# Kernel tuning notes

Measured on AMD Instinct MI355X. Metric: run time of the kernel, lower is better.

The kernel has to match this reference:

```python
import jax, jax.numpy as jnp
import numpy as np

N = 200000   # residue nodes
E = 800000   # backbone edges
P = 500000   # contact pairs to score
DIN = 128    # in_channels['res']
H = 256      # hidden per layer
L = 3        # layers


def _sage(x, src, dst, Wl, Wr, b):
    # SAGEConv: mean-aggregate source-neighbor features into dst, plus root transform
    msum = jax.ops.segment_sum(x[src], dst, num_segments=N)
    deg = jax.ops.segment_sum(jnp.ones((src.shape[0],), x.dtype), dst, num_segments=N)
    m = msum / jnp.maximum(deg, 1.0)[:, None]
    return m @ Wl + x @ Wr + b


def _graphnorm(x, w, b, ms, eps=1e-5):
    # PyG GraphNorm over a single graph (batch of all zeros)
    mu = x.mean(axis=0)
    out = x - ms * mu
    var = (out * out).mean(axis=0)
    return out / jnp.sqrt(var + eps) * w + b


def setup_inputs() -> dict:
    key = jax.random.key(0)
    ks = jax.random.split(key, 40)
    s = 0.05
    inp = {
        'x_res': jax.random.normal(ks[0], (N, DIN), jnp.float32),
        'edge_index': jax.random.randint(ks[1], (2, E), 0, N),
        'contact_pred_index': jax.random.randint(ks[2], (2, P), 0, N),
    }
    dims = [DIN, H, H]
    j = 3
    for i in range(L):
        inp['Wl%d' % i] = jax.random.normal(ks[j], (dims[i], H), jnp.float32) * s; j += 1
        inp['Wr%d' % i] = jax.random.normal(ks[j], (dims[i], H), jnp.float32) * s; j += 1
        inp['bc%d' % i] = jnp.zeros((H,), jnp.float32)
        inp['gnw%d' % i] = jnp.ones((H,), jnp.float32)
        inp['gnb%d' % i] = jnp.zeros((H,), jnp.float32)
        inp['gns%d' % i] = jnp.ones((H,), jnp.float32)
    inp['dyt_alpha'] = jnp.float32(0.5)
    inp['dyt_w'] = jnp.ones((H * L,), jnp.float32)
    inp['dyt_b'] = jnp.zeros((H * L,), jnp.float32)
    XD = [512, 512]
    inp['W1'] = jax.random.normal(ks[j], (H * L, XD[0]), jnp.float32) * s; j += 1
    inp['b1'] = jnp.zeros((XD[0],), jnp.float32)
    inp['W2'] = jax.random.normal(ks[j], (XD[0], XD[1]), jnp.float32) * s; j += 1
    inp['b2'] = jnp.zeros((XD[1],), jnp.float32)
    inp['W3'] = jax.random.normal(ks[j], (XD[1], DIN), jnp.float32) * s; j += 1
    inp['b3'] = jnp.zeros((DIN,), jnp.float32)
    CD = [256, 128]
    inp['C1'] = jax.random.normal(ks[j], (2 * DIN, CD[0]), jnp.float32) * s; j += 1
    inp['c1'] = jnp.zeros((CD[0],), jnp.float32)
    inp['C2'] = jax.random.normal(ks[j], (CD[0], CD[1]), jnp.float32) * s; j += 1
    inp['c2'] = jnp.zeros((CD[1],), jnp.float32)
    inp['C3'] = jax.random.normal(ks[j], (CD[1], 1), jnp.float32) * s; j += 1
    inp['c3'] = jnp.zeros((1,), jnp.float32)
    return inp


def reference(x_res, edge_index, contact_pred_index,
              Wl0, Wr0, bc0, gnw0, gnb0, gns0,
              Wl1, Wr1, bc1, gnw1, gnb1, gns1,
              Wl2, Wr2, bc2, gnw2, gnb2, gns2,
              dyt_alpha, dyt_w, dyt_b,
              W1, b1, W2, b2, W3, b3,
              C1, c1, C2, c2, C3, c3):
    gelu = lambda v: jax.nn.gelu(v, approximate=False)
    src, dst = edge_index[0], edge_index[1]
    inz = x_res
    h = x_res
    layers = [(Wl0, Wr0, bc0, gnw0, gnb0, gns0),
              (Wl1, Wr1, bc1, gnw1, gnb1, gns1),
              (Wl2, Wr2, bc2, gnw2, gnb2, gns2)]
    outs = []
    for i, (Wl, Wr, b, gw, gb, gs) in enumerate(layers):
        prev = h
        h = gelu(_sage(h, src, dst, Wl, Wr, b))
        h = _graphnorm(h, gw, gb, gs)
        if i > 0:
            h = h + prev
        outs.append(h)
    z = jnp.concatenate(outs, axis=1)                 # JumpingKnowledge 'cat' -> [N, 3H]
    z = jnp.tanh(dyt_alpha * z) * dyt_w + dyt_b       # DynamicTanh
    z = gelu(z @ W1 + b1)
    z = gelu(z @ W2 + b2)
    z = z @ W3 + b3
    z = z + inz                                       # residual back to input features
    z = z / (jnp.linalg.norm(z, axis=1, keepdims=True) + 1e-10)
    pair = jnp.concatenate([z[contact_pred_index[0]], z[contact_pred_index[1]]], axis=1)
    e = gelu(pair @ C1 + c1)
    e = gelu(e @ C2 + c2)
    scores = (e @ C3 + c3)[:, 0]
    return jax.nn.sigmoid(scores)
```

## Files before the change

### kernel.cpp

```cpp
#include <hip/hip_runtime.h>
#include <math.h>

typedef unsigned short u16;
typedef __attribute__((ext_vector_type(8))) short short8v;
typedef __attribute__((ext_vector_type(4))) float f32x4;

__device__ __forceinline__ float geluf(float x) {
    return 0.5f * x * (1.0f + erff(x * 0.70710678118654752f));
}
__device__ __forceinline__ float bf2f(u16 u) { return __uint_as_float((unsigned)u << 16); }
__device__ __forceinline__ u16 f2bf(float f) {
    unsigned x = __float_as_uint(f);
    unsigned r = x + 0x7FFFu + ((x >> 16) & 1u);
    return (u16)(r >> 16);
}
__device__ __forceinline__ float tanhfast(float x) {
    float cx = fminf(fmaxf(x, -15.f), 15.f);
    float t = __expf(2.f * cx);
    return (t - 1.f) / (t + 1.f);
}
__device__ __forceinline__ void gll16(const short* g, short* l) {
    __builtin_amdgcn_global_load_lds(
        (const __attribute__((address_space(1))) void*)g,
        (__attribute__((address_space(3))) void*)l, 16, 0, 0);
}

template<bool BF>
__device__ __forceinline__ float4 ld4(const void* base, long long elemOff) {
    if (BF) {
        ushort4 u = *(const ushort4*)((const u16*)base + elemOff);
        return make_float4(bf2f(u.x), bf2f(u.y), bf2f(u.z), bf2f(u.w));
    } else {
        return *(const float4*)((const float*)base + elemOff);
    }
}

__global__ __launch_bounds__(256) void cnt_kernel(const int* __restrict__ dst, int* __restrict__ cnt, int E, int Nn) {
    int e = blockIdx.x * 256 + threadIdx.x;
    if (e < E) {
        int d = dst[e];
        if ((unsigned)d < (unsigned)Nn) atomicAdd(&cnt[d], 1);
    }
}
__global__ __launch_bounds__(256) void scan1_kernel(const int* __restrict__ cnt, int* __restrict__ rp,
                                                    int* __restrict__ bs, int n) {
    __shared__ int sh[256];
    int i = blockIdx.x * 256 + threadIdx.x;
    int v = (i < n) ? cnt[i] : 0;
    sh[threadIdx.x] = v; __syncthreads();
    for (int o = 1; o < 256; o <<= 1) {
        int t = (threadIdx.x >= o) ? sh[threadIdx.x - o] : 0;
        __syncthreads();
        sh[threadIdx.x] += t;
        __syncthreads();
    }
    if (i < n) rp[i] = sh[threadIdx.x] - v;
    if (threadIdx.x == 255) bs[blockIdx.x] = sh[255];
}
__global__ __launch_bounds__(1024) void scan2_kernel(int* __restrict__ bs, int nb) {
    __shared__ int sh[1024];
    int v = (threadIdx.x < nb) ? bs[threadIdx.x] : 0;
    sh[threadIdx.x] = v; __syncthreads();
    for (int o = 1; o < 1024; o <<= 1) {
        int t = (threadIdx.x >= o) ? sh[threadIdx.x - o] : 0;
        __syncthreads();
        sh[threadIdx.x] += t;
        __syncthreads();
    }
    if (threadIdx.x < nb) bs[threadIdx.x] = sh[threadIdx.x] - v;
}
__global__ __launch_bounds__(256) void scan3_kernel(int* __restrict__ rp, int* __restrict__ cur,
                                                    const int* __restrict__ bs, int n, int E) {
    int i = blockIdx.x * 256 + threadIdx.x;
    if (i < n) {
        int v = rp[i] + bs[blockIdx.x];
        rp[i] = v;
        cur[i] = v;
    }
    if (i == 0) rp[n] = E;
}
__global__ __launch_bounds__(256) void fill_kernel(const int* __restrict__ src, const int* __restrict__ dst,
                                                   int* __restrict__ cur, int* __restrict__ srcs, int E, int Nn) {
    int e = blockIdx.x * 256 + threadIdx.x;
    if (e >= E) return;
    int d = dst[e];
    if ((unsigned)d >= (unsigned)Nn) return;
    int s = src[e];
    if ((unsigned)s >= (unsigned)Nn) s = 0;
    int p = atomicAdd(&cur[d], 1);
    srcs[p] = s;
}

template<bool L0>
__global__ __launch_bounds__(256) void agg_csr_kernel(const void* __restrict__ X, int ldx,
    const int* __restrict__ rp, const int* __restrict__ srcs,
    u16* __restrict__ m, int c0, int rows)
{
    int lrow = blockIdx.x * 4 + (threadIdx.x >> 6);
    if (lrow >= rows) return;
    int lane = threadIdx.x & 63;
    int r = c0 + lrow;
    int b = rp[r], e = rp[r + 1];
    float inv = 1.0f / fmaxf((float)(e - b), 1.0f);
    if (L0) {
        float a0 = 0.f, a1 = 0.f, c0a = 0.f, c1a = 0.f;
        int i = b;
        for (; i + 2 <= e; i += 2) {
            int s0 = srcs[i], s1 = srcs[i + 1];
            float2 v0 = *(const float2*)((const float*)X + (long long)s0 * ldx + lane * 2);
            float2 v1 = *(const float2*)((const float*)X + (long long)s1 * ldx + lane * 2);
            a0 += v0.x; a1 += v0.y;
            c0a += v1.x; c1a += v1.y;
        }
        if (i < e) {
            int s0 = srcs[i];
            float2 v0 = *(const float2*)((const float*)X + (long long)s0 * ldx + lane * 2);
            a0 += v0.x; a1 += v0.y;
        }
        a0 += c0a; a1 += c1a;
        ushort2 o; o.x = f2bf(a0 * inv); o.y = f2bf(a1 * inv);
        *(ushort2*)(m + (long long)lrow * 128 + lane * 2) = o;
    } else {
        float a0 = 0.f, a1 = 0.f, a2 = 0.f, a3 = 0.f;
        float b0 = 0.f, b1 = 0.f, b2 = 0.f, b3 = 0.f;
        int i = b;
        for (; i + 2 <= e; i += 2) {
            int s0 = srcs[i], s1 = srcs[i + 1];
            ushort4 u0 = *(const ushort4*)((const u16*)X + (long long)s0 * ldx + lane * 4);
            ushort4 u1 = *(const ushort4*)((const u16*)X + (long long)s1 * ldx + lane * 4);
            a0 += bf2f(u0.x); a1 += bf2f(u0.y); a2 += bf2f(u0.z); a3 += bf2f(u0.w);
            b0 += bf2f(u1.x); b1 += bf2f(u1.y); b2 += bf2f(u1.z); b3 += bf2f(u1.w);
        }
        if (i < e) {
            int s0 = srcs[i];
            ushort4 u0 = *(const ushort4*)((const u16*)X + (long long)s0 * ldx + lane * 4);
            a0 += bf2f(u0.x); a1 += bf2f(u0.y); a2 += bf2f(u0.z); a3 += bf2f(u0.w);
        }
        a0 += b0; a1 += b1; a2 += b2; a3 += b3;
        ushort4 o;
        o.x = f2bf(a0 * inv); o.y = f2bf(a1 * inv); o.z = f2bf(a2 * inv); o.w = f2bf(a3 * inv);
        *(ushort4*)(m + (long long)lrow * 256 + lane * 4) = o;
    }
}

struct PrepArgs {
    const float* W[11];
    short* outp[11];
    int K[11], Nc[11], kOff[11], Ktot[11];
    int start[12];
};
__global__ __launch_bounds__(256) void prep_all_kernel(PrepArgs a) {
    int idx = blockIdx.x * 256 + threadIdx.x;
    if (idx >= a.start[11]) return;
    int si = 0;
    #pragma unroll
    for (int j = 1; j < 11; ++j) si += (idx >= a.start[j]);
    int local = idx - a.start[si];
    int Nc = a.Nc[si];
    int k = local / Nc, n = local % Nc;
    a.outp[si][(long long)n * a.Ktot[si] + a.kOff[si] + k] = (short)f2bf(a.W[si][local]);
}

__device__ __forceinline__ void loadrow32(const float* p, short8v& o0, short8v& o1) {
    float4 a = *(const float4*)p;
    float4 b = *(const float4*)(p + 4);
    float4 c = *(const float4*)(p + 8);
    float4 d = *(const float4*)(p + 12);
    short8v r0, r1;
    r0[0] = (short)f2bf(a.x); r0[1] = (short)f2bf(a.y); r0[2] = (short)f2bf(a.z); r0[3] = (short)f2bf(a.w);
    r0[4] = (short)f2bf(b.x); r0[5] = (short)f2bf(b.y); r0[6] = (short)f2bf(b.z); r0[7] = (short)f2bf(b.w);
    r1[0] = (short)f2bf(c.x); r1[1] = (short)f2bf(c.y); r1[2] = (short)f2bf(c.z); r1[3] = (short)f2bf(c.w);
    r1[4] = (short)f2bf(d.x); r1[5] = (short)f2bf(d.y); r1[6] = (short)f2bf(d.z); r1[7] = (short)f2bf(d.w);
    o0 = r0; o1 = r1;
}

template<int EPI, bool A1BF, bool A2BF, bool CBF, bool STAT, bool NORM>
__global__ __launch_bounds__(256) void mm_kernel(
    const void* __restrict__ A1, int lda1,
    const void* __restrict__ A2, int lda2,
    int K1, int K2,
    const short* __restrict__ Bhi, int ldb,
    const float* __restrict__ bias,
    const float* __restrict__ resid, int ldres,
    float* __restrict__ s1, float* __restrict__ s2,
    void* __restrict__ C, int ldc, int M)
{
    __shared__ short AsL[4096];
    __shared__ short BhL[4096];
    __shared__ float cst[256];
    __shared__ float rsq[128][2];
    const int t = threadIdx.x;
    const int rowbase = blockIdx.y * 128;
    const int colbase = blockIdx.x * 128;
    const int lane = t & 63;
    const int wv = t >> 6;
    const int wr = (wv >> 1) << 6;
    const int wc = (wv & 1) << 6;
    const int l15 = lane & 15;
    const int kreg = (lane >> 4) << 3;
    const int rgrp = (lane >> 4) << 2;
    const int lr16 = lane >> 2;
    const int lchk = (lane & 3) << 3;
    const int ldsW = wv * 512;
    if (STAT && t < 256) cst[t] = 0.f;
    f32x4 acc[4][4] = {};
    const int k1t = K1 >> 5;
    const int KT = (K1 + K2) >> 5;

    for (int kt = 0; kt < KT; ++kt) {
        const bool p1 = kt < k1t;
        const int kbl = (p1 ? kt : kt - k1t) << 5;
        {
            long long kb = (long long)(kt << 5) + lchk;
            int r0 = colbase + wv * 16 + lr16;
            gll16(Bhi + (long long)r0 * ldb + kb, BhL + ldsW);
            gll16(Bhi + (long long)(r0 + 64) * ldb + kb, BhL + 2048 + ldsW);
        }
        if (p1 ? A1BF : A2BF) {
            const short* Ab = (const short*)(p1 ? A1 : A2);
            const int lda = p1 ? lda1 : lda2;
            int r0 = rowbase + wv * 16 + lr16;      if (r0 >= M) r0 = M - 1;
            int r1 = rowbase + 64 + wv * 16 + lr16; if (r1 >= M) r1 = M - 1;
            gll16(Ab + (long long)r0 * lda + kbl + lchk, AsL + ldsW);
            gll16(Ab + (long long)r1 * lda + kbl + lchk, AsL + 2048 + ldsW);
        } else {
            const float* Ab = (const float*)(p1 ? A1 : A2);
            const int lda = p1 ? lda1 : lda2;
            int row = t >> 1, half = (t & 1) << 4;
            int r = rowbase + row;
            short8v o0 = {0,0,0,0,0,0,0,0}, o1 = {0,0,0,0,0,0,0,0};
            if (r < M) loadrow32(Ab + (long long)r * lda + kbl + half, o0, o1);
            *(short8v*)&AsL[row * 32 + half]     = o0;
            *(short8v*)&AsL[row * 32 + half + 8] = o1;
        }
        __syncthreads();
        short8v a4[4], b4[4];
        #pragma unroll
        for (int mr = 0; mr < 4; ++mr)
            a4[mr] = *(short8v*)&AsL[(wr + mr * 16 + l15) * 32 + kreg];
        #pragma unroll
        for (int nr = 0; nr < 4; ++nr)
            b4[nr] = *(short8v*)&BhL[(wc + nr * 16 + l15) * 32 + kreg];
        #pragma unroll
        for (int mr = 0; mr < 4; ++mr)
            #pragma unroll
            for (int nr = 0; nr < 4; ++nr)
                acc[mr][nr] = __builtin_amdgcn_mfma_f32_16x16x32_bf16(a4[mr], b4[nr], acc[mr][nr], 0, 0, 0);
        __syncthreads();
    }

    if (NORM) {
        float rs[4][4] = {};
        #pragma unroll
        for (int nr = 0; nr < 4; ++nr) {
            int c = colbase + wc + nr * 16 + l15;
            float bi = bias[c];
            #pragma unroll
            for (int mr = 0; mr < 4; ++mr)
                #pragma unroll
                for (int i = 0; i < 4; ++i) {
                    int r = rowbase + wr + mr * 16 + rgrp + i;
                    float v = 0.f;
                    if (r < M) {
                        v = acc[mr][nr][i] + bi;
                        if (EPI == 3) v += resid[(long long)r * ldres + c];
                        if (EPI == 1) v = geluf(v);
                    }
                    acc[mr][nr][i] = v;
                    rs[mr][i] += v * v;
                }
        }
        #pragma unroll
        for (int mr = 0; mr < 4; ++mr)
            #pragma unroll
            for (int i = 0; i < 4; ++i) {
                float s = rs[mr][i];
                s += __shfl_xor(s, 1); s += __shfl_xor(s, 2);
                s += __shfl_xor(s, 4); s += __shfl_xor(s, 8);
                rs[mr][i] = s;
            }
        if (l15 == 0) {
            #pragma unroll
            for (int mr = 0; mr < 4; ++mr)
                #pragma unroll
                for (int i = 0; i < 4; ++i)
                    rsq[wr + mr * 16 + rgrp + i][wv & 1] = rs[mr][i];
        }
        __syncthreads();
        #pragma unroll
        for (int mr = 0; mr < 4; ++mr)
            #pragma unroll
            for (int i = 0; i < 4; ++i) {
                int rl = wr + mr * 16 + rgrp + i;
                int r = rowbase + rl;
                if (r >= M) continue;
                float inv = 1.0f / (sqrtf(rsq[rl][0] + rsq[rl][1]) + 1e-10f);
                #pragma unroll
                for (int nr = 0; nr < 4; ++nr) {
                    int c = colbase + wc + nr * 16 + l15;
                    float v = acc[mr][nr][i] * inv;
                    if (CBF) ((u16*)C)[(long long)r * ldc + c] = f2bf(v);
                    else     ((float*)C)[(long long)r * ldc + c] = v;
                }
            }
    } else {
        #pragma unroll
        for (int nr = 0; nr < 4; ++nr) {
            int c = colbase + wc + nr * 16 + l15;
            float bi = bias[c];
            float cp = 0.f, cq = 0.f;
            #pragma unroll
            for (int mr = 0; mr < 4; ++mr)
                #pragma unroll
                for (int i = 0; i < 4; ++i) {
                    int r = rowbase + wr + mr * 16 + rgrp + i;
                    if (r >= M) continue;
                    float v = acc[mr][nr][i] + bi;
                    if (EPI == 1) v = geluf(v);
                    if (EPI == 3) v += resid[(long long)r * ldres + c];
                    if (CBF) ((u16*)C)[(long long)r * ldc + c] = f2bf(v);
                    else     ((float*)C)[(long long)r * ldc + c] = v;
                    if (STAT) { cp += v; cq += v * v; }
                }
            if (STAT) {
                cp += __shfl_xor(cp, 16); cp += __shfl_xor(cp, 32);
                cq += __shfl_xor(cq, 16); cq += __shfl_xor(cq, 32);
                if (lane < 16) {
                    int cl = wc + nr * 16 + l15;
                    atomicAdd(&cst[cl], cp);
                    atomicAdd(&cst[128 + cl], cq);
                }
            }
        }
        if (STAT) {
            __syncthreads();
            if (t < 128) {
                atomicAdd(s1 + colbase + t, cst[t]);
                atomicAdd(s2 + colbase + t, cst[128 + t]);
            }
        }
    }
}

__global__ __launch_bounds__(256) void pair_kernel(
    const u16* __restrict__ zf,
    const int* __restrict__ g1, const int* __restrict__ g2,
    int Nn, int P,
    const short* __restrict__ C1t, const float* __restrict__ c1,
    const short* __restrict__ C2t, const float* __restrict__ c2,
    const float* __restrict__ C3, const float* __restrict__ c3,
    float* __restrict__ out)
{
    __shared__ short E1s[64 * 264];
    __shared__ float sc[64][2];
    const int t = threadIdx.x;
    const int lane = t & 63;
    const int wv = t >> 6;
    const int wr = (wv >> 1) << 5;
    const int wc = (wv & 1) << 6;
    const int l15 = lane & 15;
    const int kreg = (lane >> 4) << 3;
    const int rgrp = (lane >> 4) << 2;
    const int p0 = blockIdx.x * 64;

    int gidx[2][2];
    #pragma unroll
    for (int mr = 0; mr < 2; ++mr) {
        int pr = p0 + wr + mr * 16 + l15;
        int a = (pr < P) ? g1[pr] : 0;  if ((unsigned)a >= (unsigned)Nn) a = 0;
        gidx[0][mr] = a;
        int b = (pr < P) ? g2[pr] : 0;  if ((unsigned)b >= (unsigned)Nn) b = 0;
        gidx[1][mr] = b;
    }

    short8v az[2][2][4];
    #pragma unroll
    for (int half = 0; half < 2; ++half)
        #pragma unroll
        for (int mr = 0; mr < 2; ++mr)
            #pragma unroll
            for (int ktl = 0; ktl < 4; ++ktl)
                az[half][mr][ktl] = *(const short8v*)((const short*)zf
                    + (long long)gidx[half][mr] * 128 + (ktl << 5) + kreg);

    #pragma unroll
    for (int ch = 0; ch < 2; ++ch) {
        f32x4 acc1[2][4] = {};
        #pragma unroll
        for (int kt = 0; kt < 8; ++kt) {
            const int half = kt >> 2;
            const int ktl = kt & 3;
            short8v b4[4];
            #pragma unroll
            for (int nr = 0; nr < 4; ++nr)
                b4[nr] = *(const short8v*)(C1t + (long long)(ch * 128 + wc + nr * 16 + l15) * 256 + (kt << 5) + kreg);
            #pragma unroll
            for (int mr = 0; mr < 2; ++mr)
                #pragma unroll
                for (int nr = 0; nr < 4; ++nr)
                    acc1[mr][nr] = __builtin_amdgcn_mfma_f32_16x16x32_bf16(az[half][mr][ktl], b4[nr], acc1[mr][nr], 0, 0, 0);
        }
        #pragma unroll
        for (int nr = 0; nr < 4; ++nr) {
            int cc = wc + nr * 16 + l15;
            float bi = c1[ch * 128 + cc];
            #pragma unroll
            for (int mr = 0; mr < 2; ++mr)
                #pragma unroll
                for (int i = 0; i < 4; ++i) {
                    float v = geluf(acc1[mr][nr][i] + bi);
                    E1s[(wr + mr * 16 + rgrp + i) * 264 + ch * 128 + cc] = (short)f2bf(v);
                }
        }
    }
    __syncthreads();

    f32x4 acc[2][4] = {};
    #pragma unroll
    for (int kt = 0; kt < 8; ++kt) {
        short8v a4[2], b4[4];
        #pragma unroll
        for (int mr = 0; mr < 2; ++mr)
            a4[mr] = *(short8v*)&E1s[(wr + mr * 16 + l15) * 264 + (kt << 5) + kreg];
        #pragma unroll
        for (int nr = 0; nr < 4; ++nr)
            b4[nr] = *(const short8v*)(C2t + (long long)(wc + nr * 16 + l15) * 256 + (kt << 5) + kreg);
        #pragma unroll
        for (int mr = 0; mr < 2; ++mr)
            #pragma unroll
            for (int nr = 0; nr < 4; ++nr)
                acc[mr][nr] = __builtin_amdgcn_mfma_f32_16x16x32_bf16(a4[mr], b4[nr], acc[mr][nr], 0, 0, 0);
    }

    float pr_[2][4] = {};
    #pragma unroll
    for (int nr = 0; nr < 4; ++nr) {
        int cc = wc + nr * 16 + l15;
        float bi = c2[cc];
        float w3 = C3[cc];
        #pragma unroll
        for (int mr = 0; mr < 2; ++mr)
            #pragma unroll
            for (int i = 0; i < 4; ++i)
                pr_[mr][i] += geluf(acc[mr][nr][i] + bi) * w3;
    }
    #pragma unroll
    for (int mr = 0; mr < 2; ++mr)
        #pragma unroll
        for (int i = 0; i < 4; ++i) {
            float s = pr_[mr][i];
            s += __shfl_xor(s, 1); s += __shfl_xor(s, 2);
            s += __shfl_xor(s, 4); s += __shfl_xor(s, 8);
            pr_[mr][i] = s;
        }
    if (l15 == 0) {
        #pragma unroll
        for (int mr = 0; mr < 2; ++mr)
            #pragma unroll
            for (int i = 0; i < 4; ++i)
                sc[wr + mr * 16 + rgrp + i][wv & 1] = pr_[mr][i];
    }
    __syncthreads();
    if (t < 64) {
        int p = p0 + t;
        if (p < P) {
            float x = sc[t][0] + sc[t][1] + c3[0];
            out[p] = 1.0f / (1.0f + expf(-x));
        }
    }
}

template<bool DYT>
__global__ __launch_bounds__(256) void gn_apply_kernel(u16* __restrict__ G, int ldg,
    const u16* __restrict__ prev, int ldp, int M,
    const float* __restrict__ s1, const float* __restrict__ s2,
    const float* __restrict__ gw, const float* __restrict__ gb, const float* __restrict__ gs,
    float invN,
    const float* __restrict__ dA, const float* __restrict__ dW, const float* __restrict__ dB)
{
    long long idx = (long long)blockIdx.x * blockDim.x + threadIdx.x;
    if (idx >= (long long)M * 64) return;
    int c0 = (int)(idx & 63) << 2;
    long long r = idx >> 6;
    float4 g = ld4<true>(G, r * ldg + c0);
    float o[4] = {g.x, g.y, g.z, g.w};
    float alpha = DYT ? dA[0] : 0.f;
    #pragma unroll
    for (int j = 0; j < 4; ++j) {
        int c = c0 + j;
        float mu = s1[c] * invN;
        float ms = gs[c];
        float var = s2[c] * invN - mu * mu * ms * (2.0f - ms);
        float rstd = rsqrtf(var + 1e-5f);
        o[j] = (o[j] - ms * mu) * rstd * gw[c] + gb[c];
    }
    if (prev) {
        float4 pv = ld4<true>(prev, r * ldp + c0);
        o[0] += pv.x; o[1] += pv.y; o[2] += pv.z; o[3] += pv.w;
    }
    if (DYT) {
        #pragma unroll
        for (int j = 0; j < 4; ++j)
            o[j] = tanhfast(alpha * o[j]) * dW[c0 + j] + dB[c0 + j];
    }
    ushort4 u; u.x = f2bf(o[0]); u.y = f2bf(o[1]); u.z = f2bf(o[2]); u.w = f2bf(o[3]);
    *(ushort4*)((u16*)G + r * ldg + c0) = u;
}

__global__ __launch_bounds__(256) void dyt512_kernel(u16* __restrict__ Z,
    const float* __restrict__ alphaP, const float* __restrict__ w, const float* __restrict__ b,
    long long total)
{
    long long idx = (long long)blockIdx.x * blockDim.x + threadIdx.x;
    if (idx >= total) return;
    int c0 = (int)(idx & 63) << 3;
    long long r = idx >> 6;
    float alpha = alphaP[0];
    short8v z = *(short8v*)(Z + r * 768 + c0);
    float4 w0 = *(const float4*)(w + c0);
    float4 w1 = *(const float4*)(w + c0 + 4);
    float4 b0 = *(const float4*)(b + c0);
    float4 b1 = *(const float4*)(b + c0 + 4);
    short8v o;
    o[0] = (short)f2bf(tanhfast(alpha * bf2f((u16)z[0])) * w0.x + b0.x);
    o[1] = (short)f2bf(tanhfast(alpha * bf2f((u16)z[1])) * w0.y + b0.y);
    o[2] = (short)f2bf(tanhfast(alpha * bf2f((u16)z[2])) * w0.z + b0.z);
    o[3] = (short)f2bf(tanhfast(alpha * bf2f((u16)z[3])) * w0.w + b0.w);
    o[4] = (short)f2bf(tanhfast(alpha * bf2f((u16)z[4])) * w1.x + b1.x);
    o[5] = (short)f2bf(tanhfast(alpha * bf2f((u16)z[5])) * w1.y + b1.y);
    o[6] = (short)f2bf(tanhfast(alpha * bf2f((u16)z[6])) * w1.z + b1.z);
    o[7] = (short)f2bf(tanhfast(alpha * bf2f((u16)z[7])) * w1.w + b1.w);
    *(short8v*)(Z + r * 768 + c0) = o;
}

extern "C" void kernel_launch(void* const* d_in, const int* in_sizes, int n_in,
                              void* d_out, int out_size, void* d_ws, size_t ws_size,
                              hipStream_t stream) {
    const float* x_res = (const float*)d_in[0];
    const int* eidx = (const int*)d_in[1];
    const int* cidx = (const int*)d_in[2];
    const int N = in_sizes[0] / 128;
    const int E = in_sizes[1] / 2;
    const int P = in_sizes[2] / 2;
    const int* src = eidx;
    const int* dst = eidx + E;
    const int* g1 = cidx;
    const int* g2 = cidx + P;
    const float* Wl[3] = {(const float*)d_in[3], (const float*)d_in[9],  (const float*)d_in[15]};
    const float* Wr[3] = {(const float*)d_in[4], (const float*)d_in[10], (const float*)d_in[16]};
    const float* bc[3] = {(const float*)d_in[5], (const float*)d_in[11], (const float*)d_in[17]};
    const float* gnw[3] = {(const float*)d_in[6], (const float*)d_in[12], (const float*)d_in[18]};
    const float* gnb[3] = {(const float*)d_in[7], (const float*)d_in[13], (const float*)d_in[19]};
    const float* gns[3] = {(const float*)d_in[8], (const float*)d_in[14], (const float*)d_in[20]};
    const float* alphaP = (const float*)d_in[21];
    const float* dytw = (const float*)d_in[22];
    const float* dytb = (const float*)d_in[23];
    const float* W1 = (const float*)d_in[24]; const float* b1 = (const float*)d_in[25];
    const float* W2 = (const float*)d_in[26]; const float* b2 = (const float*)d_in[27];
    const float* W3 = (const float*)d_in[28]; const float* b3 = (const float*)d_in[29];
    const float* C1 = (const float*)d_in[30]; const float* c1 = (const float*)d_in[31];
    const float* C2 = (const float*)d_in[32]; const float* c2 = (const float*)d_in[33];
    const float* C3 = (const float*)d_in[34]; const float* c3 = (const float*)d_in[35];
    float* out = (float*)d_out;

    char* ws = (char*)d_ws;
    size_t off = 0;
    size_t zOff  = off; off += (size_t)N * 768 * 2;     off = (off + 255) & ~(size_t)255;
    size_t stOff = off; off += 4096;                    off = (off + 255) & ~(size_t)255;
    size_t zfOff = off; off += (size_t)N * 128 * 2;     off = (off + 255) & ~(size_t)255;
    size_t rpOff = off; off += (size_t)(N + 1) * 4;     off = (off + 255) & ~(size_t)255;
    size_t curOff = off; off += (size_t)N * 4;          off = (off + 255) & ~(size_t)255;
    size_t srcsOff = off; off += (size_t)E * 4;         off = (off + 255) & ~(size_t)255;
    size_t bsOff = off; off += 4096;                    off = (off + 255) & ~(size_t)255;
    static const size_t se[8] = {65536, 131072, 131072, 393216, 262144, 65536, 65536, 32768};
    short* wt[8];
    for (int i = 0; i < 8; ++i) {
        wt[i] = (short*)(ws + off);
        off += 2 * se[i];
        off = (off + 255) & ~(size_t)255;
    }
    size_t pOff = off;
    size_t avail = ws_size > pOff ? ws_size - pOff : 0;

    u16*   Z    = (u16*)(ws + zOff);
    float* st   = (float*)(ws + stOff);
    u16*   zf   = (u16*)(ws + zfOff);
    int*   rp   = (int*)(ws + rpOff);
    int*   cur  = (int*)(ws + curOff);
    int*   srcs = (int*)(ws + srcsOff);
    int*   bs   = (int*)(ws + bsOff);
    u16*   pbuf = (u16*)(ws + pOff);

    int NC = (int)((avail /  512) & ~(size_t)127); if (NC < 128) NC = 128; if (NC > N) NC = N;
    int S  = (int)((avail / 2048) & ~(size_t)127); if (S  < 128) S  = 128; if (S  > N) S  = N;

    dim3 blk(256);

    {
        PrepArgs a;
        const float* Ws[11] = {Wl[0], Wr[0], Wl[1], Wr[1], Wl[2], Wr[2], W1, W2, W3, C1, C2};
        short* Os[11] = {wt[0], wt[0], wt[1], wt[1], wt[2], wt[2], wt[3], wt[4], wt[5], wt[6], wt[7]};
        int Ks[11]    = {128, 128, 256, 256, 256, 256, 768, 512, 512, 256, 256};
        int Ncs[11]   = {256, 256, 256, 256, 256, 256, 512, 512, 128, 256, 128};
        int kOffs[11] = {0, 128, 0, 256, 0, 256, 0, 0, 0, 0, 0};
        int Ktots[11] = {256, 256, 512, 512, 512, 512, 768, 512, 512, 256, 256};
        int s = 0;
        for (int i = 0; i < 11; ++i) {
            a.W[i] = Ws[i]; a.outp[i] = Os[i];
            a.K[i] = Ks[i]; a.Nc[i] = Ncs[i]; a.kOff[i] = kOffs[i]; a.Ktot[i] = Ktots[i];
            a.start[i] = s;
            s += Ks[i] * Ncs[i];
        }
        a.start[11] = s;
        prep_all_kernel<<<(s + 255) / 256, 256, 0, stream>>>(a);
    }

    int nb = (N + 255) / 256;
    hipMemsetAsync(cur, 0, (size_t)N * 4, stream);
    cnt_kernel<<<(E + 255) / 256, 256, 0, stream>>>(dst, cur, E, N);
    scan1_kernel<<<nb, 256, 0, stream>>>(cur, rp, bs, N);
    scan2_kernel<<<1, 1024, 0, stream>>>(bs, nb);
    scan3_kernel<<<nb, 256, 0, stream>>>(rp, cur, bs, N, E);
    fill_kernel<<<(E + 255) / 256, 256, 0, stream>>>(src, dst, cur, srcs, E, N);

    u16* m = pbuf;
    for (int l = 0; l < 3; ++l) {
        u16* Zl = Z + l * 256;
        hipMemsetAsync(st, 0, 512 * 4, stream);
        for (int c0 = 0; c0 < N; c0 += NC) {
            int rows = (N - c0 < NC) ? (N - c0) : NC;
            int aggblocks = (rows + 3) / 4;
            dim3 grid(2, (rows + 127) / 128);
            if (l == 0) {
                agg_csr_kernel<true><<<aggblocks, 256, 0, stream>>>(x_res, 128, rp, srcs, m, c0, rows);
                mm_kernel<1, true, false, true, true, false><<<grid, blk, 0, stream>>>(
                    m, 128, x_res + (size_t)c0 * 128, 128, 128, 128,
                    wt[0], 256, bc[0], nullptr, 0, st, st + 256,
                    Zl + (size_t)c0 * 768, 768, rows);
            } else {
                const u16* h = Z + (l - 1) * 256;
                agg_csr_kernel<false><<<aggblocks, 256, 0, stream>>>(h, 768, rp, srcs, m, c0, rows);
                mm_kernel<1, true, true, true, true, false><<<grid, blk, 0, stream>>>(
                    m, 256, h + (size_t)c0 * 768, 768, 256, 256,
                    wt[l], 512, bc[l], nullptr, 0, st, st + 256,
                    Zl + (size_t)c0 * 768, 768, rows);
            }
        }
        const u16* prev = (l == 0) ? nullptr : (Z + (l - 1) * 256);
        int gnblocks = (int)(((long long)N * 64 + 255) / 256);
        if (l == 2)
            gn_apply_kernel<true><<<gnblocks, 256, 0, stream>>>(
                Zl, 768, prev, 768, N, st, st + 256, gnw[l], gnb[l], gns[l], 1.0f / (float)N,
                alphaP, dytw + 512, dytb + 512);
        else
            gn_apply_kernel<false><<<gnblocks, 256, 0, stream>>>(
                Zl, 768, prev, 768, N, st, st + 256, gnw[l], gnb[l], gns[l], 1.0f / (float)N,
                nullptr, nullptr, nullptr);
    }

    dyt512_kernel<<<(int)(((long long)N * 64 + 255) / 256), 256, 0, stream>>>(
        Z, alphaP, dytw, dytb, (long long)N * 64);

    {
        short* t1c = (short*)pbuf;
        short* t2c = t1c + (size_t)S * 512;
        for (int r0 = 0; r0 < N; r0 += S) {
            int rows = (N - r0 < S) ? (N - r0) : S;
            mm_kernel<1, true, true, true, false, false><<<dim3(4, (rows + 127) / 128), blk, 0, stream>>>(
                Z + (size_t)r0 * 768, 768, nullptr, 0, 768, 0,
                wt[3], 768, b1, nullptr, 0, nullptr, nullptr, t1c, 512, rows);
            mm_kernel<1, true, true, true, false, false><<<dim3(4, (rows + 127) / 128), blk, 0, stream>>>(
                t1c, 512, nullptr, 0, 512, 0,
                wt[4], 512, b2, nullptr, 0, nullptr, nullptr, t2c, 512, rows);
            mm_kernel<3, true, true, true, false, true><<<dim3(1, (rows + 127) / 128), blk, 0, stream>>>(
                t2c, 512, nullptr, 0, 512, 0,
                wt[5], 512, b3, x_res + (size_t)r0 * 128, 128, nullptr, nullptr,
                zf + (size_t)r0 * 128, 128, rows);
        }
    }

    pair_kernel<<<(P + 63) / 64, blk, 0, stream>>>(
        zf, g1, g2, N, P, wt[6], c1, wt[7], c2, C3, c3, out);
}
```

Measured before the change: 3.189 ms.

## Unroll CSR aggregation to 4 edges and XOR-swizzle GEMM LDS tiles

The neighbour-mean aggregation kernels now process four source rows per iteration with independent accumulators, so more gathers are in flight per wave. The GEMM kernel's LDS tiles get an XOR swizzle of the 16-byte k-chunk by row, applied on both the global-to-LDS loads and the fragment reads, to reduce LDS bank conflicts. The swizzle must match exactly on write and read paths; the unroll adds register pressure.

```diff
diff --git a/kernel.cpp b/kernel.cpp
--- a/kernel.cpp
+++ b/kernel.cpp
@@ -103,40 +103,52 @@
     int b = rp[r], e = rp[r + 1];
     float inv = 1.0f / fmaxf((float)(e - b), 1.0f);
     if (L0) {
-        float a0 = 0.f, a1 = 0.f, c0a = 0.f, c1a = 0.f;
+        float a0 = 0.f, a1 = 0.f, b0 = 0.f, b1 = 0.f;
+        float c0a = 0.f, c1a = 0.f, d0 = 0.f, d1 = 0.f;
         int i = b;
-        for (; i + 2 <= e; i += 2) {
-            int s0 = srcs[i], s1 = srcs[i + 1];
+        for (; i + 4 <= e; i += 4) {
+            int s0 = srcs[i], s1 = srcs[i + 1], s2 = srcs[i + 2], s3 = srcs[i + 3];
             float2 v0 = *(const float2*)((const float*)X + (long long)s0 * ldx + lane * 2);
             float2 v1 = *(const float2*)((const float*)X + (long long)s1 * ldx + lane * 2);
+            float2 v2 = *(const float2*)((const float*)X + (long long)s2 * ldx + lane * 2);
+            float2 v3 = *(const float2*)((const float*)X + (long long)s3 * ldx + lane * 2);
             a0 += v0.x; a1 += v0.y;
-            c0a += v1.x; c1a += v1.y;
-        }
-        if (i < e) {
+            b0 += v1.x; b1 += v1.y;
+            c0a += v2.x; c1a += v2.y;
+            d0 += v3.x; d1 += v3.y;
+        }
+        for (; i < e; ++i) {
             int s0 = srcs[i];
             float2 v0 = *(const float2*)((const float*)X + (long long)s0 * ldx + lane * 2);
             a0 += v0.x; a1 += v0.y;
         }
-        a0 += c0a; a1 += c1a;
+        a0 += b0 + c0a + d0; a1 += b1 + c1a + d1;
         ushort2 o; o.x = f2bf(a0 * inv); o.y = f2bf(a1 * inv);
         *(ushort2*)(m + (long long)lrow * 128 + lane * 2) = o;
     } else {
         float a0 = 0.f, a1 = 0.f, a2 = 0.f, a3 = 0.f;
         float b0 = 0.f, b1 = 0.f, b2 = 0.f, b3 = 0.f;
+        float c0_ = 0.f, c1_ = 0.f, c2_ = 0.f, c3_ = 0.f;
+        float d0 = 0.f, d1 = 0.f, d2 = 0.f, d3 = 0.f;
         int i = b;
-        for (; i + 2 <= e; i += 2) {
-            int s0 = srcs[i], s1 = srcs[i + 1];
+        for (; i + 4 <= e; i += 4) {
+            int s0 = srcs[i], s1 = srcs[i + 1], s2 = srcs[i + 2], s3 = srcs[i + 3];
             ushort4 u0 = *(const ushort4*)((const u16*)X + (long long)s0 * ldx + lane * 4);
             ushort4 u1 = *(const ushort4*)((const u16*)X + (long long)s1 * ldx + lane * 4);
+            ushort4 u2 = *(const ushort4*)((const u16*)X + (long long)s2 * ldx + lane * 4);
+            ushort4 u3 = *(const ushort4*)((const u16*)X + (long long)s3 * ldx + lane * 4);
             a0 += bf2f(u0.x); a1 += bf2f(u0.y); a2 += bf2f(u0.z); a3 += bf2f(u0.w);
             b0 += bf2f(u1.x); b1 += bf2f(u1.y); b2 += bf2f(u1.z); b3 += bf2f(u1.w);
-        }
-        if (i < e) {
+            c0_ += bf2f(u2.x); c1_ += bf2f(u2.y); c2_ += bf2f(u2.z); c3_ += bf2f(u2.w);
+            d0 += bf2f(u3.x); d1 += bf2f(u3.y); d2 += bf2f(u3.z); d3 += bf2f(u3.w);
+        }
+        for (; i < e; ++i) {
             int s0 = srcs[i];
             ushort4 u0 = *(const ushort4*)((const u16*)X + (long long)s0 * ldx + lane * 4);
             a0 += bf2f(u0.x); a1 += bf2f(u0.y); a2 += bf2f(u0.z); a3 += bf2f(u0.w);
         }
-        a0 += b0; a1 += b1; a2 += b2; a3 += b3;
+        a0 += b0 + c0_ + d0; a1 += b1 + c1_ + d1;
+        a2 += b2 + c2_ + d2; a3 += b3 + c3_ + d3;
         ushort4 o;
         o.x = f2bf(a0 * inv); o.y = f2bf(a1 * inv); o.z = f2bf(a2 * inv); o.w = f2bf(a3 * inv);
         *(ushort4*)(m + (long long)lrow * 256 + lane * 4) = o;
@@ -200,8 +212,9 @@
     const int kreg = (lane >> 4) << 3;
     const int rgrp = (lane >> 4) << 2;
     const int lr16 = lane >> 2;
-    const int lchk = (lane & 3) << 3;
+    const int swz = (((lane & 3) ^ (lr16 & 3)) << 3);
     const int ldsW = wv * 512;
+    const int rdk = (((lane >> 4) ^ (l15 & 3)) << 3);
     if (STAT && t < 256) cst[t] = 0.f;
     f32x4 acc[4][4] = {};
     const int k1t = K1 >> 5;
@@ -211,7 +224,7 @@
         const bool p1 = kt < k1t;
         const int kbl = (p1 ? kt : kt - k1t) << 5;
         {
-            long long kb = (long long)(kt << 5) + lchk;
+            long long kb = (long long)(kt << 5) + swz;
             int r0 = colbase + wv * 16 + lr16;
             gll16(Bhi + (long long)r0 * ldb + kb, BhL + ldsW);
             gll16(Bhi + (long long)(r0 + 64) * ldb + kb, BhL + 2048 + ldsW);
@@ -221,26 +234,26 @@
             const int lda = p1 ? lda1 : lda2;
             int r0 = rowbase + wv * 16 + lr16;      if (r0 >= M) r0 = M - 1;
             int r1 = rowbase + 64 + wv * 16 + lr16; if (r1 >= M) r1 = M - 1;
-            gll16(Ab + (long long)r0 * lda + kbl + lchk, AsL + ldsW);
-            gll16(Ab + (long long)r1 * lda + kbl + lchk, AsL + 2048 + ldsW);
+            gll16(Ab + (long long)r0 * lda + kbl + swz, AsL + ldsW);
+            gll16(Ab + (long long)r1 * lda + kbl + swz, AsL + 2048 + ldsW);
         } else {
             const float* Ab = (const float*)(p1 ? A1 : A2);
             const int lda = p1 ? lda1 : lda2;
-            int row = t >> 1, half = (t & 1) << 4;
+            int row = t >> 1, h = (t & 1) << 1;
             int r = rowbase + row;
             short8v o0 = {0,0,0,0,0,0,0,0}, o1 = {0,0,0,0,0,0,0,0};
-            if (r < M) loadrow32(Ab + (long long)r * lda + kbl + half, o0, o1);
-            *(short8v*)&AsL[row * 32 + half]     = o0;
-            *(short8v*)&AsL[row * 32 + half + 8] = o1;
+            if (r < M) loadrow32(Ab + (long long)r * lda + kbl + (h << 3), o0, o1);
+            *(short8v*)&AsL[row * 32 + ((h ^ (row & 3)) << 3)]       = o0;
+            *(short8v*)&AsL[row * 32 + (((h + 1) ^ (row & 3)) << 3)] = o1;
         }
         __syncthreads();
         short8v a4[4], b4[4];
         #pragma unroll
         for (int mr = 0; mr < 4; ++mr)
-            a4[mr] = *(short8v*)&AsL[(wr + mr * 16 + l15) * 32 + kreg];
+            a4[mr] = *(short8v*)&AsL[(wr + mr * 16 + l15) * 32 + rdk];
         #pragma unroll
         for (int nr = 0; nr < 4; ++nr)
-            b4[nr] = *(short8v*)&BhL[(wc + nr * 16 + l15) * 32 + kreg];
+            b4[nr] = *(short8v*)&BhL[(wc + nr * 16 + l15) * 32 + rdk];
         #pragma unroll
         for (int mr = 0; mr < 4; ++mr)
             #pragma unroll
```

New measurement: 3.189 ms. Within noise of the previous version (-0.0%).
